# Kernel optimization log

Measured on AMD Instinct MI355X. Metric: run time of the kernel, lower is better.

Reference implementation:

```python
import jax, jax.numpy as jnp
import numpy as np

N_NODES = 100000
N_EDGES = 640000
D_IN = 128
D_OUT = 128


def setup_inputs() -> dict:
    key = jax.random.key(0)
    k1, k2, k3, k4, k5, k6 = jax.random.split(key, 6)
    x = jax.random.normal(k1, (N_NODES, D_IN), dtype=jnp.float32)
    edge_weights = jax.random.uniform(k2, (N_EDGES, 1), dtype=jnp.float32)
    src = jax.random.randint(k3, (N_EDGES,), 0, N_NODES)
    dst = jax.random.randint(k4, (N_EDGES,), 0, N_NODES)
    # nn.Linear init scale ~ 1/sqrt(in_feats)
    W = jax.random.normal(k5, (D_OUT, D_IN), dtype=jnp.float32) / np.sqrt(D_IN)
    b = jax.random.normal(k6, (D_OUT,), dtype=jnp.float32) / np.sqrt(D_IN)
    return {"x": x, "edge_weights": edge_weights, "src": src, "dst": dst, "W": W, "b": b}


def reference(x, edge_weights, src, dst, W, b):
    # message: gather source node features, scale by per-edge weight  [E, D]
    m = x[src] * edge_weights
    # reduce: sum messages into destination nodes  [N, D]
    h = jax.ops.segment_sum(m, dst, num_segments=N_NODES)
    # dense linear  [N, D_OUT]
    return h @ W.T + b
```

## Files before the change

### kernel.cpp

```cpp
#include <hip/hip_runtime.h>
#include <hip/hip_bf16.h>

#define D 128
#define SCAN_CH 4096

typedef __bf16 bf16x8 __attribute__((ext_vector_type(8)));
typedef float  f32x4  __attribute__((ext_vector_type(4)));
typedef float  f32x2  __attribute__((ext_vector_type(2)));

__device__ __forceinline__ __bf16 f2bf(float f) { return (__bf16)f; }
__device__ __forceinline__ int pad8(int v) { return (v + 7) & ~7; }

__global__ __launch_bounds__(256) void pack_w_kernel(
    const float* __restrict__ W, __bf16* __restrict__ wb,
    int* __restrict__ cnt, int M)
{
    int t = blockIdx.x * 256 + threadIdx.x;
    for (int i = t; i < M; i += gridDim.x * 256) cnt[i] = 0;

    if (t < 2048) {
        int lane = t & 63;
        int frag = t >> 6;
        int kb = frag >> 3, fn = frag & 7;
        int n  = fn * 16 + (lane & 15);
        int k0 = kb * 32 + (lane >> 4) * 8;
        const float* src = &W[(size_t)n * D + k0];
        float4 v0 = *reinterpret_cast<const float4*>(src);
        float4 v1 = *reinterpret_cast<const float4*>(src + 4);
        bf16x8 o;
        o[0]=f2bf(v0.x); o[1]=f2bf(v0.y); o[2]=f2bf(v0.z); o[3]=f2bf(v0.w);
        o[4]=f2bf(v1.x); o[5]=f2bf(v1.y); o[6]=f2bf(v1.z); o[7]=f2bf(v1.w);
        *reinterpret_cast<bf16x8*>(&wb[((size_t)frag * 64 + lane) * 8]) = o;
    }
}

__global__ __launch_bounds__(256) void gemm_mfma_kernel(
    const float* __restrict__ x, const __bf16* __restrict__ wb,
    __bf16* __restrict__ y, int M)
{
    const int tid  = threadIdx.x;
    const int lane = tid & 63;
    const int wv   = tid >> 6;
    const int l15  = lane & 15;
    const int l4   = lane >> 4;
    const int row_base = blockIdx.x * 128 + wv * 32;

    f32x4 acc[2][8];
    #pragma unroll
    for (int mi = 0; mi < 2; ++mi)
        #pragma unroll
        for (int fn = 0; fn < 8; ++fn)
            #pragma unroll
            for (int c = 0; c < 4; ++c) acc[mi][fn][c] = 0.f;

    #pragma unroll
    for (int kb = 0; kb < 4; ++kb) {
        bf16x8 b[8];
        #pragma unroll
        for (int fn = 0; fn < 8; ++fn)
            b[fn] = *reinterpret_cast<const bf16x8*>(
                        &wb[((size_t)(kb * 8 + fn) * 64 + lane) * 8]);
        #pragma unroll
        for (int mi = 0; mi < 2; ++mi) {
            int row = row_base + mi * 16 + l15;
            int rc  = row < M ? row : M - 1;
            const f32x4* ap = reinterpret_cast<const f32x4*>(
                                   &x[(size_t)rc * D + kb * 32 + l4 * 8]);
            f32x4 v0 = __builtin_nontemporal_load(ap);
            f32x4 v1 = __builtin_nontemporal_load(ap + 1);
            bf16x8 a;
            a[0]=f2bf(v0[0]); a[1]=f2bf(v0[1]); a[2]=f2bf(v0[2]); a[3]=f2bf(v0[3]);
            a[4]=f2bf(v1[0]); a[5]=f2bf(v1[1]); a[6]=f2bf(v1[2]); a[7]=f2bf(v1[3]);
            #pragma unroll
            for (int fn = 0; fn < 8; ++fn)
                acc[mi][fn] = __builtin_amdgcn_mfma_f32_16x16x32_bf16(
                                  a, b[fn], acc[mi][fn], 0, 0, 0);
        }
    }

    #pragma unroll
    for (int mi = 0; mi < 2; ++mi)
        #pragma unroll
        for (int r = 0; r < 4; ++r) {
            int row = row_base + mi * 16 + l4 * 4 + r;
            if (row >= M) continue;
            #pragma unroll
            for (int fn = 0; fn < 8; ++fn)
                y[(size_t)row * D + fn * 16 + l15] = f2bf(acc[mi][fn][r]);
        }
}

__global__ __launch_bounds__(256) void hist_kernel(
    const int* __restrict__ dst, int* __restrict__ cnt,
    int* __restrict__ rank, int E)
{
    int e = blockIdx.x * 256 + threadIdx.x;
    if (e < E) {
        int d = __builtin_nontemporal_load(&dst[e]);
        rank[e] = atomicAdd(&cnt[d], 1);
    }
}

__global__ __launch_bounds__(256) void scan_part_kernel(
    const int* __restrict__ cnt, int* __restrict__ bsum, int N)
{
    __shared__ int wred[4];
    const int tid  = threadIdx.x;
    const int lane = tid & 63;
    const int wid  = tid >> 6;
    int off = blockIdx.x * SCAN_CH + tid * 16;
    int s = 0;
    #pragma unroll
    for (int i = 0; i < 16; ++i) {
        int idx = off + i;
        if (idx < N) s += pad8(cnt[idx]);
    }
    #pragma unroll
    for (int d = 32; d >= 1; d >>= 1) s += __shfl_xor(s, d, 64);
    if (lane == 0) wred[wid] = s;
    __syncthreads();
    if (tid == 0) bsum[blockIdx.x] = wred[0] + wred[1] + wred[2] + wred[3];
}

__global__ __launch_bounds__(256) void scan_write_kernel(
    const int* __restrict__ cnt, const int* __restrict__ bsum,
    int* __restrict__ base, int N, int NB)
{
    __shared__ int boff_s;
    __shared__ int wsum[4];
    const int b    = blockIdx.x;
    const int tid  = threadIdx.x;
    const int lane = tid & 63;
    const int wid  = tid >> 6;

    if (wid == 0) {
        int v = (lane < b) ? bsum[lane] : 0;
        #pragma unroll
        for (int d = 32; d >= 1; d >>= 1) v += __shfl_xor(v, d, 64);
        if (lane == 0) boff_s = v;
    }
    __syncthreads();

    int off = b * SCAN_CH + tid * 16;
    int v[16];
    int s = 0;
    #pragma unroll
    for (int i = 0; i < 16; ++i) {
        int idx = off + i;
        v[i] = (idx < N) ? pad8(cnt[idx]) : 0;
        s += v[i];
    }
    int ssum = s;
    #pragma unroll
    for (int d = 1; d < 64; d <<= 1) {
        int t = __shfl_up(ssum, d, 64);
        if (lane >= d) ssum += t;
    }
    if (lane == 63) wsum[wid] = ssum;
    __syncthreads();
    int woff = 0;
    for (int w = 0; w < wid; ++w) woff += wsum[w];

    int run = boff_s + woff + ssum - s;
    #pragma unroll
    for (int i = 0; i < 16; ++i) {
        int idx = off + i;
        if (idx < N) base[idx] = run;
        if (idx == N - 1) base[N] = run + v[i];
        run += v[i];
    }
}

__global__ __launch_bounds__(256) void bin_kernel(
    const int* __restrict__ src, const int* __restrict__ dst,
    const float* __restrict__ ew, const int* __restrict__ base,
    const int* __restrict__ rank, int2* __restrict__ bins, int E)
{
    int e = blockIdx.x * 256 + threadIdx.x;
    if (e >= E) return;
    int d  = __builtin_nontemporal_load(&dst[e]);
    int sv = __builtin_nontemporal_load(&src[e]);
    float w = __builtin_nontemporal_load(&ew[e]);
    int rk = __builtin_nontemporal_load(&rank[e]);
    int p = base[d] + rk;
    bins[p] = make_int2(sv * (D / 2), __float_as_int(w));
}

__global__ __launch_bounds__(256) void gather_kernel(
    const __bf16* __restrict__ y, const int* __restrict__ base,
    const int2* __restrict__ bins, const float* __restrict__ bias,
    float* __restrict__ out, int N)
{
    int gw   = (blockIdx.x * 256 + threadIdx.x) >> 6;
    int lane = threadIdx.x & 63;
    if (gw >= N) return;

    const unsigned* yb = reinterpret_cast<const unsigned*>(y);
    int b0 = base[gw], b1 = base[gw + 1];
    float accx = 0.f, accy = 0.f;

    for (int i = b0; i < b1; i += 8) {
        int2 e[8];
        #pragma unroll
        for (int t = 0; t < 8; ++t) e[t] = bins[i + t];
        unsigned p[8];
        #pragma unroll
        for (int t = 0; t < 8; ++t)
            p[t] = yb[(unsigned)e[t].x + lane];
        #pragma unroll
        for (int t = 0; t < 8; ++t) {
            float w = __int_as_float(e[t].y);
            accx += __uint_as_float(p[t] << 16) * w;
            accy += __uint_as_float(p[t] & 0xFFFF0000u) * w;
        }
    }

    float2 bv = *reinterpret_cast<const float2*>(&bias[lane * 2]);
    f32x2 o;
    o[0] = accx + bv.x;
    o[1] = accy + bv.y;
    __builtin_nontemporal_store(o, reinterpret_cast<f32x2*>(&out[(size_t)gw * D + lane * 2]));
}

extern "C" void kernel_launch(void* const* d_in, const int* in_sizes, int n_in,
                              void* d_out, int out_size, void* d_ws, size_t ws_size,
                              hipStream_t stream) {
    const float* x   = (const float*)d_in[0];
    const float* ew  = (const float*)d_in[1];
    const int*   src = (const int*)d_in[2];
    const int*   dst = (const int*)d_in[3];
    const float* W   = (const float*)d_in[4];
    const float* b   = (const float*)d_in[5];
    float*       out = (float*)d_out;

    const int E  = in_sizes[2];
    const int M  = out_size / D;
    const int NB = (M + SCAN_CH - 1) / SCAN_CH;
    const size_t BIN_CAP = (size_t)E + 7 * (size_t)M + 8;

    char* p = (char*)d_ws;
    __bf16* y    = (__bf16*)p;             p += (size_t)M * D * 2;
    __bf16* wb   = (__bf16*)p;             p += (size_t)32 * 64 * 8 * 2;
    int2*   bins = (int2*)p;               p += BIN_CAP * 8;
    int*    base = (int*)p;                p += (size_t)(M + 1) * 4;
    int*    cnt  = (int*)p;                p += (size_t)M * 4;
    int*    rank = (int*)p;                p += (size_t)E * 4;
    int*    bsum = (int*)p;

    (void)hipMemsetAsync(bins, 0, BIN_CAP * sizeof(int2), stream);

    pack_w_kernel<<<64, 256, 0, stream>>>(W, wb, cnt, M);

    gemm_mfma_kernel<<<(M + 127) / 128, 256, 0, stream>>>(x, wb, y, M);

    hist_kernel<<<(E + 255) / 256, 256, 0, stream>>>(dst, cnt, rank, E);
    scan_part_kernel<<<NB, 256, 0, stream>>>(cnt, bsum, M);
    scan_write_kernel<<<NB, 256, 0, stream>>>(cnt, bsum, base, M, NB);
    bin_kernel<<<(E + 255) / 256, 256, 0, stream>>>(src, dst, ew, base, rank, bins, E);

    gather_kernel<<<(M * 64 + 255) / 256, 256, 0, stream>>>(y, base, bins, b, out, M);
}
```

Before: 131.9 us.

## Replace atomic-rank binning with two-pass bucketed counting sort fused into GEMM launch

Swaps the global per-edge atomic rank and scatter binning for a two-level counting sort. Edges are first bucketed into coarse blocks of 512 destination nodes using shared-memory histograms, with that pass fused into the GEMM launch so it can overlap. A per-bucket pass then places edges using shared-memory atomics and zeroes the padding itself, which removes the full bins memset. The cost is extra intermediate buffers (cDst, cSW) and a second scatter pass, while the global atomics per edge are kept in the histogram pass.

```diff
diff --git a/kernel.cpp b/kernel.cpp
--- a/kernel.cpp
+++ b/kernel.cpp
@@ -3,6 +3,8 @@
 
 #define D 128
 #define SCAN_CH 4096
+#define NP1 256
+#define BSH 9
 
 typedef __bf16 bf16x8 __attribute__((ext_vector_type(8)));
 typedef float  f32x4  __attribute__((ext_vector_type(4)));
@@ -11,7 +13,7 @@
 __device__ __forceinline__ __bf16 f2bf(float f) { return (__bf16)f; }
 __device__ __forceinline__ int pad8(int v) { return (v + 7) & ~7; }
 
-__global__ __launch_bounds__(256) void pack_w_kernel(
+__global__ __launch_bounds__(256) void prep_kernel(
     const float* __restrict__ W, __bf16* __restrict__ wb,
     int* __restrict__ cnt, int M)
 {
@@ -34,16 +36,37 @@
     }
 }
 
-__global__ __launch_bounds__(256) void gemm_mfma_kernel(
+__global__ __launch_bounds__(256) void gemm_p1a_kernel(
     const float* __restrict__ x, const __bf16* __restrict__ wb,
-    __bf16* __restrict__ y, int M)
-{
-    const int tid  = threadIdx.x;
+    __bf16* __restrict__ y, int M,
+    const int* __restrict__ dst, int* __restrict__ cnt,
+    int* __restrict__ cnts, int E, int chunk, int NBK)
+{
+    __shared__ int h[256];
+    const int tid = threadIdx.x;
+
+    if (blockIdx.x < NP1) {
+        h[tid] = 0;
+        __syncthreads();
+        int s = blockIdx.x * chunk;
+        int e = s + chunk < E ? s + chunk : E;
+        for (int i = s + tid; i < e; i += 256) {
+            int d = dst[i];
+            atomicAdd(&cnt[d], 1);
+            atomicAdd(&h[d >> BSH], 1);
+        }
+        __syncthreads();
+        if (tid < NBK) cnts[(size_t)tid * NP1 + blockIdx.x] = h[tid];
+        return;
+    }
+
+    const int gb   = blockIdx.x - NP1;
     const int lane = tid & 63;
     const int wv   = tid >> 6;
     const int l15  = lane & 15;
     const int l4   = lane >> 4;
-    const int row_base = blockIdx.x * 128 + wv * 32;
+    const int row_base = gb * 128 + wv * 32;
+    if (row_base >= M) return;
 
     f32x4 acc[2][8];
     #pragma unroll
@@ -90,64 +113,63 @@
         }
 }
 
-__global__ __launch_bounds__(256) void hist_kernel(
-    const int* __restrict__ dst, int* __restrict__ cnt,
-    int* __restrict__ rank, int E)
-{
-    int e = blockIdx.x * 256 + threadIdx.x;
-    if (e < E) {
-        int d = __builtin_nontemporal_load(&dst[e]);
-        rank[e] = atomicAdd(&cnt[d], 1);
-    }
-}
-
-__global__ __launch_bounds__(256) void scan_part_kernel(
-    const int* __restrict__ cnt, int* __restrict__ bsum, int N)
+__global__ __launch_bounds__(256) void scan2_part_kernel(
+    const int* __restrict__ cnt, int N,
+    const int* __restrict__ cnts, int NC,
+    int* __restrict__ bsumA, int* __restrict__ bsumB, int NB_A)
 {
     __shared__ int wred[4];
     const int tid  = threadIdx.x;
     const int lane = tid & 63;
     const int wid  = tid >> 6;
-    int off = blockIdx.x * SCAN_CH + tid * 16;
+    const bool A   = (int)blockIdx.x < NB_A;
+    const int blk  = A ? blockIdx.x : blockIdx.x - NB_A;
+    int off = blk * SCAN_CH + tid * 16;
     int s = 0;
     #pragma unroll
     for (int i = 0; i < 16; ++i) {
         int idx = off + i;
-        if (idx < N) s += pad8(cnt[idx]);
+        if (A) { if (idx < N)  s += pad8(cnt[idx]); }
+        else   { if (idx < NC) s += cnts[idx]; }
     }
     #pragma unroll
     for (int d = 32; d >= 1; d >>= 1) s += __shfl_xor(s, d, 64);
     if (lane == 0) wred[wid] = s;
     __syncthreads();
-    if (tid == 0) bsum[blockIdx.x] = wred[0] + wred[1] + wred[2] + wred[3];
-}
-
-__global__ __launch_bounds__(256) void scan_write_kernel(
-    const int* __restrict__ cnt, const int* __restrict__ bsum,
-    int* __restrict__ base, int N, int NB)
+    if (tid == 0) (A ? bsumA : bsumB)[blk] = wred[0] + wred[1] + wred[2] + wred[3];
+}
+
+__global__ __launch_bounds__(256) void scan2_write_kernel(
+    const int* __restrict__ cnt, int N, int* __restrict__ base,
+    const int* __restrict__ bsumA,
+    const int* __restrict__ cnts, int NC, int* __restrict__ coffs,
+    const int* __restrict__ bsumB, int NB_A)
 {
     __shared__ int boff_s;
     __shared__ int wsum[4];
-    const int b    = blockIdx.x;
     const int tid  = threadIdx.x;
     const int lane = tid & 63;
     const int wid  = tid >> 6;
+    const bool A   = (int)blockIdx.x < NB_A;
+    const int blk  = A ? blockIdx.x : blockIdx.x - NB_A;
 
     if (wid == 0) {
-        int v = (lane < b) ? bsum[lane] : 0;
+        const int* bs = A ? bsumA : bsumB;
+        int v = (lane < blk) ? bs[lane] : 0;
         #pragma unroll
         for (int d = 32; d >= 1; d >>= 1) v += __shfl_xor(v, d, 64);
         if (lane == 0) boff_s = v;
     }
     __syncthreads();
 
-    int off = b * SCAN_CH + tid * 16;
+    int off = blk * SCAN_CH + tid * 16;
     int v[16];
     int s = 0;
     #pragma unroll
     for (int i = 0; i < 16; ++i) {
         int idx = off + i;
-        v[i] = (idx < N) ? pad8(cnt[idx]) : 0;
+        if (A) v[i] = (idx < N)  ? pad8(cnt[idx]) : 0;
+        else   v[i] = (idx < NC) ? cnts[idx] : 0;
         s += v[i];
     }
     int ssum = s;
@@ -165,25 +187,69 @@
     #pragma unroll
     for (int i = 0; i < 16; ++i) {
         int idx = off + i;
-        if (idx < N) base[idx] = run;
-        if (idx == N - 1) base[N] = run + v[i];
+        if (A) {
+            if (idx < N) base[idx] = run;
+            if (idx == N - 1) base[N] = run + v[i];
+        } else {
+            if (idx < NC) coffs[idx] = run;
+        }
         run += v[i];
     }
 }
 
-__global__ __launch_bounds__(256) void bin_kernel(
+__global__ __launch_bounds__(256) void p1b_kernel(
     const int* __restrict__ src, const int* __restrict__ dst,
-    const float* __restrict__ ew, const int* __restrict__ base,
-    const int* __restrict__ rank, int2* __restrict__ bins, int E)
-{
-    int e = blockIdx.x * 256 + threadIdx.x;
-    if (e >= E) return;
-    int d  = __builtin_nontemporal_load(&dst[e]);
-    int sv = __builtin_nontemporal_load(&src[e]);
-    float w = __builtin_nontemporal_load(&ew[e]);
-    int rk = __builtin_nontemporal_load(&rank[e]);
-    int p = base[d] + rk;
-    bins[p] = make_int2(sv * (D / 2), __float_as_int(w));
+    const float* __restrict__ ew, const int* __restrict__ coffs,
+    int* __restrict__ cDst, int2* __restrict__ cSW, int E, int chunk, int NBK)
+{
+    __shared__ int h[256];
+    const int tid = threadIdx.x;
+    const int k   = blockIdx.x;
+    if (tid < NBK) h[tid] = coffs[(size_t)tid * NP1 + k];
+    __syncthreads();
+    int s = k * chunk;
+    int e = s + chunk < E ? s + chunk : E;
+    for (int i = s + tid; i < e; i += 256) {
+        int d  = dst[i];
+        int p  = atomicAdd(&h[d >> BSH], 1);
+        cDst[p] = d;
+        cSW[p]  = make_int2(src[i] * (D / 2), __float_as_int(ew[i]));
+    }
+}
+
+__global__ __launch_bounds__(256) void p2_kernel(
+    const int* __restrict__ cDst, const int2* __restrict__ cSW,
+    const int* __restrict__ coffs, const int* __restrict__ base,
+    int2* __restrict__ bins, int M, int E, int NBK)
+{
+    __shared__ int cur[512];
+    const int tid = threadIdx.x;
+    const int b   = blockIdx.x;
+    const int n0  = b << BSH;
+
+    for (int ld = tid; ld < 512; ld += 256) {
+        int n = n0 + ld;
+        cur[ld] = (n < M) ? base[n] : 0;
+    }
+    __syncthreads();
+
+    int e0 = coffs[(size_t)b * NP1];
+    int e1 = (b + 1 < NBK) ? coffs[(size_t)(b + 1) * NP1] : E;
+    for (int i = e0 + tid; i < e1; i += 256) {
+        int ld = cDst[i] & 511;
+        int p  = atomicAdd(&cur[ld], 1);
+        bins[p] = cSW[i];
+    }
+    __syncthreads();
+
+    const int2 z = make_int2(0, 0);
+    for (int ld = tid; ld < 512; ld += 256) {
+        int n = n0 + ld;
+        if (n < M) {
+            int end = base[n + 1];
+            for (int p = cur[ld]; p < end; ++p) bins[p] = z;
+        }
+    }
 }
 
 __global__ __launch_bounds__(256) void gather_kernel(
@@ -196,7 +262,8 @@
     if (gw >= N) return;
 
     const unsigned* yb = reinterpret_cast<const unsigned*>(y);
-    int b0 = base[gw], b1 = base[gw + 1];
+    const int b0 = __builtin_amdgcn_readfirstlane(base[gw]);
+    const int b1 = __builtin_amdgcn_readfirstlane(base[gw + 1]);
     float accx = 0.f, accy = 0.f;
 
     for (int i = b0; i < b1; i += 8) {
@@ -233,30 +300,42 @@
     const float* b   = (const float*)d_in[5];
     float*       out = (float*)d_out;
 
-    const int E  = in_sizes[2];
-    const int M  = out_size / D;
-    const int NB = (M + SCAN_CH - 1) / SCAN_CH;
+    const int E     = in_sizes[2];
+    const int M     = out_size / D;
+    const int NBK   = (M + 511) >> BSH;
+    const int NC    = NBK * NP1;
+    const int chunk = (E + NP1 - 1) / NP1;
+    const int NB_A  = (M + SCAN_CH - 1) / SCAN_CH;
+    const int NB_B  = (NC + SCAN_CH - 1) / SCAN_CH;
     const size_t BIN_CAP = (size_t)E + 7 * (size_t)M + 8;
 
     char* p = (char*)d_ws;
-    __bf16* y    = (__bf16*)p;             p += (size_t)M * D * 2;
-    __bf16* wb   = (__bf16*)p;             p += (size_t)32 * 64 * 8 * 2;
-    int2*   bins = (int2*)p;               p += BIN_CAP * 8;
-    int*    base = (int*)p;                p += (size_t)(M + 1) * 4;
-    int*    cnt  = (int*)p;                p += (size_t)M * 4;
-    int*    rank = (int*)p;                p += (size_t)E * 4;
-    int*    bsum = (int*)p;
-
-    (void)hipMemsetAsync(bins, 0, BIN_CAP * sizeof(int2), stream);
-
-    pack_w_kernel<<<64, 256, 0, stream>>>(W, wb, cnt, M);
-
-    gemm_mfma_kernel<<<(M + 127) / 128, 256, 0, stream>>>(x, wb, y, M);
-
-    hist_kernel<<<(E + 255) / 256, 256, 0, stream>>>(dst, cnt, rank, E);
-    scan_part_kernel<<<NB, 256, 0, stream>>>(cnt, bsum, M);
-    scan_write_kernel<<<NB, 256, 0, stream>>>(cnt, bsum, base, M, NB);
-    bin_kernel<<<(E + 255) / 256, 256, 0, stream>>>(src, dst, ew, base, rank, bins, E);
+    __bf16* y     = (__bf16*)p;            p += (size_t)M * D * 2;
+    __bf16* wb    = (__bf16*)p;            p += (size_t)32 * 64 * 8 * 2;
+    int2*   bins  = (int2*)p;              p += BIN_CAP * 8;
+    int*    base  = (int*)p;               p += (size_t)(M + 1) * 4;
+    int*    cnt   = (int*)p;               p += (size_t)M * 4;
+    int*    cnts  = (int*)p;               p += (size_t)NC * 4;
+    int*    coffs = (int*)p;               p += (size_t)NC * 4;
+    int*    cDst  = (int*)p;               p += (size_t)E * 4;
+    int2*   cSW   = (int2*)p;              p += (size_t)E * 8;
+    int*    bsumA = (int*)p;               p += 64 * 4;
+    int*    bsumB = (int*)p;
+
+    prep_kernel<<<64, 256, 0, stream>>>(W, wb, cnt, M);
+
+    int gemmBlocks = (M + 127) / 128;
+    gemm_p1a_kernel<<<NP1 + gemmBlocks, 256, 0, stream>>>(
+        x, wb, y, M, dst, cnt, cnts, E, chunk, NBK);
+
+    scan2_part_kernel<<<NB_A + NB_B, 256, 0, stream>>>(
+        cnt, M, cnts, NC, bsumA, bsumB, NB_A);
+    scan2_write_kernel<<<NB_A + NB_B, 256, 0, stream>>>(
+        cnt, M, base, bsumA, cnts, NC, coffs, bsumB, NB_A);
+
+    p1b_kernel<<<NP1, 256, 0, stream>>>(src, dst, ew, coffs, cDst, cSW, E, chunk, NBK);
+
+    p2_kernel<<<NBK, 256, 0, stream>>>(cDst, cSW, coffs, base, bins, M, E, NBK);
 
     gather_kernel<<<(M * 64 + 255) / 256, 256, 0, stream>>>(y, base, bins, b, out, M);
 }
```

Result: faster. 122.3 us (-7.3%).
